# Kernel optimization log

Hardware: AMD Instinct MI355X
Metric: run time of the kernel (lower is better)

Reference implementation:

```python
import jax, jax.numpy as jnp
import numpy as np

B, T, D = 4, 4096, 1024


def setup_inputs() -> dict:
    key = jax.random.key(0)
    ks = jax.random.split(key, 10)
    scale = 1.0 / np.sqrt(D)
    x = jax.random.normal(ks[0], (B, T, D), jnp.float32)
    last_x = jnp.zeros((D,), jnp.float32)
    last_num = jnp.zeros((D,), jnp.float32)
    last_den = jnp.zeros((D,), jnp.float32)
    time_decay = jax.random.normal(ks[1], (D,), jnp.float32) * 0.1
    time_first = jax.random.normal(ks[2], (D,), jnp.float32) * 0.1
    time_mix_k = jax.random.uniform(ks[3], (1, 1, D), jnp.float32)
    time_mix_v = jax.random.uniform(ks[4], (1, 1, D), jnp.float32)
    time_mix_r = jax.random.uniform(ks[5], (1, 1, D), jnp.float32)
    Wk = jax.random.normal(ks[6], (D, D), jnp.float32) * scale
    Wv = jax.random.normal(ks[7], (D, D), jnp.float32) * scale
    Wr = jax.random.normal(ks[8], (D, D), jnp.float32) * scale
    Wo = jax.random.normal(ks[9], (D, D), jnp.float32) * scale
    return {"x": x, "last_x": last_x, "last_num": last_num, "last_den": last_den,
            "time_decay": time_decay, "time_first": time_first,
            "time_mix_k": time_mix_k, "time_mix_v": time_mix_v, "time_mix_r": time_mix_r,
            "Wk": Wk, "Wv": Wv, "Wr": Wr, "Wo": Wo}


def reference(x, last_x, last_num, last_den, time_decay, time_first,
              time_mix_k, time_mix_v, time_mix_r, Wk, Wv, Wr, Wo):
    # token-shift lerps against the incoming state (broadcast over B, T)
    k = jnp.einsum('btd,ed->bte', x * time_mix_k + last_x * (1.0 - time_mix_k), Wk)
    v = jnp.einsum('btd,ed->bte', x * time_mix_v + last_x * (1.0 - time_mix_v), Wv)
    r = jnp.einsum('btd,ed->bte', x * time_mix_r + last_x * (1.0 - time_mix_r), Wr)
    # WKV numerics, exactly as the original (no extra stabilization)
    efk = jnp.exp(time_first + k)          # exp(time_first + k), [B,T,D]
    wkv = (last_num + efk * v) / (last_den + efk)
    rwkv = jax.nn.sigmoid(r) * wkv
    decay = jnp.exp(-jnp.exp(time_decay))  # [D]
    ek = jnp.exp(k)
    num = decay * last_num + ek * v
    den = decay * last_den + ek
    out = jnp.einsum('btd,ed->bte', rwkv, Wo)
    return out, x[..., -1, :], num[..., -1, :], den[..., -1, :]
```

## Files before the change

### kernel.cpp

```cpp
#include <hip/hip_runtime.h>
#include <cstdint>
#include <cstddef>

constexpr int DD = 1024;
constexpr int TT = 4096;
constexpr int BB = 4;
constexpr int MM = BB * TT;

typedef __bf16 bf16x8 __attribute__((ext_vector_type(8)));
typedef float  f32x4  __attribute__((ext_vector_type(4)));

__device__ __forceinline__ unsigned short f2bf(float f) {
  union { float f; uint32_t u; } c; c.f = f;
  uint32_t r = (c.u + 0x7FFFu + ((c.u >> 16) & 1u)) >> 16;
  return (unsigned short)r;
}

__device__ __forceinline__ float fast_rcp(float x) {
  return __builtin_amdgcn_rcpf(x);
}

__device__ __forceinline__ void async_ld16(const unsigned short* g, unsigned short* lds_dst) {
  __builtin_amdgcn_global_load_lds(
      (const __attribute__((address_space(1))) void*)g,
      (__attribute__((address_space(3))) void*)lds_dst,
      16, 0, 0);
}

__global__ void prep_all(const float* __restrict__ Wk, const float* __restrict__ Wv,
                         const float* __restrict__ Wr, const float* __restrict__ Wo,
                         const float* __restrict__ tmk, const float* __restrict__ tmv,
                         const float* __restrict__ tmr,
                         const float* __restrict__ last_x,
                         const float4* __restrict__ x,
                         unsigned short* __restrict__ wz,
                         unsigned short* __restrict__ wo,
                         float* __restrict__ bias,
                         ushort4* __restrict__ xb,
                         float4* __restrict__ out_xlast) {
  if (blockIdx.x < 1024) {
    int w = (blockIdx.x * 256 + threadIdx.x) >> 6;
    int lane = threadIdx.x & 63;
    int z = w >> 10;
    int e = w & (DD - 1);
    const float* W  = (z == 0) ? Wk  : (z == 1) ? Wv  : (z == 2) ? Wr : Wo;
    const float* tm = (z == 0) ? tmk : (z == 1) ? tmv : tmr;
    unsigned short* dst = (z < 3) ? (wz + (size_t)z * DD * DD + (size_t)e * DD)
                                  : (wo + (size_t)e * DD);
    float s = 0.f;
#pragma unroll
    for (int j = 0; j < 4; ++j) {
      int d = j * 256 + lane * 4;
      float4 wv4 = *(const float4*)(W + (size_t)e * DD + d);
      if (z < 3) {
        float4 t4 = *(const float4*)(tm + d);
        float4 l4 = *(const float4*)(last_x + d);
        s += l4.x * (1.f - t4.x) * wv4.x + l4.y * (1.f - t4.y) * wv4.y +
             l4.z * (1.f - t4.z) * wv4.z + l4.w * (1.f - t4.w) * wv4.w;
        wv4.x *= t4.x; wv4.y *= t4.y; wv4.z *= t4.z; wv4.w *= t4.w;
      }
      ushort4 o;
      o.x = f2bf(wv4.x); o.y = f2bf(wv4.y); o.z = f2bf(wv4.z); o.w = f2bf(wv4.w);
      *(ushort4*)(dst + d) = o;
    }
    if (z < 3) {
      for (int off = 32; off; off >>= 1) s += __shfl_down(s, off, 64);
      if (lane == 0) bias[z * DD + e] = s;
    }
  } else {
    int i = (blockIdx.x - 1024) * 256 + threadIdx.x;
    float4 v = x[i];
    ushort4 o;
    o.x = f2bf(v.x); o.y = f2bf(v.y); o.z = f2bf(v.z); o.w = f2bf(v.w);
    xb[i] = o;
    int m = i >> 8;
    if ((m & (TT - 1)) == (TT - 1)) {
      int b = m >> 12;
      out_xlast[b * 256 + (i & 255)] = v;
    }
  }
}

__global__ __launch_bounds__(256, 2) void gemm_kvr(
    const unsigned short* __restrict__ A,
    const unsigned short* __restrict__ Wz,
    const float* __restrict__ bias,
    const float* __restrict__ time_first, const float* __restrict__ time_decay,
    const float* __restrict__ last_num, const float* __restrict__ last_den,
    unsigned short* __restrict__ rwkv,
    float* __restrict__ out_num, float* __restrict__ out_den) {
  __shared__ unsigned short lA[2][128 * 32];
  __shared__ unsigned short lB[2][3][64 * 32];
  const int tid  = threadIdx.x;
  const int lane = tid & 63;
  const int wave = tid >> 6;

  const int id  = blockIdx.y * gridDim.x + blockIdx.x;
  const int xcd = id & 7;
  const int s   = id >> 3;
  const int m0 = (xcd * 16 + (s >> 4)) * 128;
  const int n0 = (s & 15) * 64;

  const int wm = (wave >> 1) * 64;
  const int wn = (wave & 1) * 32;

  f32x4 acc[3][4][2] = {};

  const int fr_row = lane & 15;
  const int fr_kb  = (lane >> 4) * 16;
  const int srow = tid >> 2;
  const int scol = (tid & 3) * 8;

  for (int k0 = 0; k0 < DD; k0 += 64) {
    __syncthreads();
#pragma unroll
    for (int h = 0; h < 2; ++h) {
      int kk = k0 + h * 32;
#pragma unroll
      for (int it = 0; it < 2; ++it) {
        int cc  = it * 256 + tid;
        int row = cc >> 2;
        async_ld16(A + (size_t)(m0 + row) * DD + (kk + scol),
                   lA[h] + (size_t)(it * 256 + wave * 64) * 8);
      }
#pragma unroll
      for (int z = 0; z < 3; ++z) {
        async_ld16(Wz + (size_t)z * DD * DD + (size_t)(n0 + srow) * DD + (kk + scol),
                   lB[h][z] + (size_t)(wave * 64) * 8);
      }
    }
    __syncthreads();

#pragma unroll
    for (int h = 0; h < 2; ++h) {
      bf16x8 af[4], bfr[3][2];
#pragma unroll
      for (int i = 0; i < 4; ++i)
        af[i] = *(const bf16x8*)((const char*)lA[h] + ((wm + i * 16 + fr_row) * 64 + fr_kb));
#pragma unroll
      for (int z = 0; z < 3; ++z)
#pragma unroll
        for (int j = 0; j < 2; ++j)
          bfr[z][j] = *(const bf16x8*)((const char*)lB[h][z] + ((wn + j * 16 + fr_row) * 64 + fr_kb));

#pragma unroll
      for (int mi = 0; mi < 4; ++mi)
#pragma unroll
        for (int z = 0; z < 3; ++z)
#pragma unroll
          for (int ni = 0; ni < 2; ++ni)
            acc[z][mi][ni] = __builtin_amdgcn_mfma_f32_16x16x32_bf16(
                af[mi], bfr[z][ni], acc[z][mi][ni], 0, 0, 0);
    }
  }

  const int crow = (lane >> 4) * 4;
  const int ccol = lane & 15;
#pragma unroll
  for (int ni = 0; ni < 2; ++ni) {
    int gnz = n0 + wn + ni * 16 + ccol;
    float bk = bias[gnz], bv = bias[DD + gnz], br = bias[2 * DD + gnz];
    float tf = time_first[gnz];
    float ln = last_num[gnz], ld = last_den[gnz];
    float dec = __expf(-__expf(time_decay[gnz]));
#pragma unroll
    for (int mi = 0; mi < 4; ++mi) {
#pragma unroll
      for (int r = 0; r < 4; ++r) {
        int gm = m0 + wm + mi * 16 + crow + r;
        float kk = acc[0][mi][ni][r] + bk;
        float vv = acc[1][mi][ni][r] + bv;
        float rr = acc[2][mi][ni][r] + br;
        float efk = __expf(tf + kk);
        float wkv = (ln + efk * vv) * fast_rcp(ld + efk);
        float sr  = fast_rcp(1.0f + __expf(-rr));
        rwkv[(size_t)gm * DD + gnz] = f2bf(sr * wkv);
        if ((gm & (TT - 1)) == (TT - 1)) {
          int b = gm >> 12;
          float ek = __expf(kk);
          out_num[b * DD + gnz] = dec * ln + ek * vv;
          out_den[b * DD + gnz] = dec * ld + ek;
        }
      }
    }
  }
}

__global__ void gemm_bt128(const unsigned short* __restrict__ A,
                           const unsigned short* __restrict__ Bw,
                           float* __restrict__ Cf,
                           int M, int N, int K) {
  __shared__ unsigned short lA[2][128 * 32];
  __shared__ unsigned short lB[2][128 * 32];
  const int tid  = threadIdx.x;
  const int lane = tid & 63;
  const int wave = tid >> 6;

  const int nBlocks = N >> 7;
  const int mBlocks = M >> 7;
  const int id  = blockIdx.y * gridDim.x + blockIdx.x;
  const int xcd = id & 7;
  const int s   = id >> 3;
  const int mPer = mBlocks >> 3;
  const int m0 = (xcd * mPer + s / nBlocks) * 128;
  const int n0 = (s % nBlocks) * 128;

  const int wm = (wave >> 1) * 64;
  const int wn = (wave & 1) * 64;

  f32x4 acc[4][4] = {};
  const int fr_row = lane & 15;
  const int fr_kb  = (lane >> 4) * 16;
  const int scol = (tid & 3) * 8;

  for (int k0 = 0; k0 < K; k0 += 64) {
    __syncthreads();
#pragma unroll
    for (int h = 0; h < 2; ++h) {
      int kk = k0 + h * 32;
#pragma unroll
      for (int it = 0; it < 2; ++it) {
        int cc  = it * 256 + tid;
        int row = cc >> 2;
        async_ld16(A + (size_t)(m0 + row) * K + (kk + scol),
                   lA[h] + (size_t)(it * 256 + wave * 64) * 8);
      }
#pragma unroll
      for (int it = 0; it < 2; ++it) {
        int cc  = it * 256 + tid;
        int row = cc >> 2;
        async_ld16(Bw + (size_t)(n0 + row) * K + (kk + scol),
                   lB[h] + (size_t)(it * 256 + wave * 64) * 8);
      }
    }
    __syncthreads();

#pragma unroll
    for (int h = 0; h < 2; ++h) {
      bf16x8 af[4], bfr[4];
#pragma unroll
      for (int i = 0; i < 4; ++i) {
        af[i]  = *(const bf16x8*)((const char*)lA[h] + ((wm + i * 16 + fr_row) * 64 + fr_kb));
        bfr[i] = *(const bf16x8*)((const char*)lB[h] + ((wn + i * 16 + fr_row) * 64 + fr_kb));
      }
#pragma unroll
      for (int mi = 0; mi < 4; ++mi)
#pragma unroll
        for (int ni = 0; ni < 4; ++ni)
          acc[mi][ni] = __builtin_amdgcn_mfma_f32_16x16x32_bf16(af[mi], bfr[ni], acc[mi][ni], 0, 0, 0);
    }
  }

  const int crow = (lane >> 4) * 4;
  const int ccol = lane & 15;
#pragma unroll
  for (int mi = 0; mi < 4; ++mi) {
#pragma unroll
    for (int ni = 0; ni < 4; ++ni) {
      int gn = n0 + wn + ni * 16 + ccol;
#pragma unroll
      for (int r = 0; r < 4; ++r) {
        int gm = m0 + wm + mi * 16 + crow + r;
        Cf[(size_t)gm * N + gn] = acc[mi][ni][r];
      }
    }
  }
}

extern "C" void kernel_launch(void* const* d_in, const int* in_sizes, int n_in,
                              void* d_out, int out_size, void* d_ws, size_t ws_size,
                              hipStream_t stream) {
  const float* x          = (const float*)d_in[0];
  const float* last_x     = (const float*)d_in[1];
  const float* last_num   = (const float*)d_in[2];
  const float* last_den   = (const float*)d_in[3];
  const float* time_decay = (const float*)d_in[4];
  const float* time_first = (const float*)d_in[5];
  const float* tmk        = (const float*)d_in[6];
  const float* tmv        = (const float*)d_in[7];
  const float* tmr        = (const float*)d_in[8];
  const float* Wk         = (const float*)d_in[9];
  const float* Wv         = (const float*)d_in[10];
  const float* Wr         = (const float*)d_in[11];
  const float* Wo         = (const float*)d_in[12];

  float* out       = (float*)d_out;
  float* out_xlast = out + (size_t)MM * DD;
  float* out_num   = out_xlast + BB * DD;
  float* out_den   = out_num + BB * DD;

  char* ws = (char*)d_ws;
  unsigned short* xb   = (unsigned short*)ws;
  unsigned short* wz   = (unsigned short*)(ws + 33554432);
  unsigned short* wo   = (unsigned short*)(ws + 39845888);
  float*          bias = (float*)(ws + 41943040);
  unsigned short* rwkv = (unsigned short*)(ws + 41955328);

  prep_all<<<1024 + MM * DD / 4 / 256, 256, 0, stream>>>(
      Wk, Wv, Wr, Wo, tmk, tmv, tmr, last_x, (const float4*)x,
      wz, wo, bias, (ushort4*)xb, (float4*)out_xlast);

  gemm_kvr<<<dim3(DD / 64, MM / 128), 256, 0, stream>>>(
      xb, wz, bias, time_first, time_decay, last_num, last_den,
      rwkv, out_num, out_den);

  gemm_bt128<<<dim3(DD / 128, MM / 128), 256, 0, stream>>>(
      rwkv, wo, out, MM, DD, DD);
}
```

Before: 291.5 us.

## Restructure fused KVR GEMM with 512-thread 256-row tiles, swizzled LDS, double-buffered pipeline

The fused k/v/r GEMM moves from 256-thread blocks with 128-row tiles to 512-thread blocks with 256-row tiles. It uses XOR-swizzled LDS layouts to avoid bank conflicts and double-buffers the global-to-LDS async loads so the next k-slice is prefetched while the MFMAs run. The MFMA phases are split per projection, with s_setprio and explicit barriers and waitcnts. The aim is to hide memory latency and reduce LDS conflicts. In exchange, LDS use is larger, register pressure is higher, and the hand-placed synchronisation is fragile.

```diff
diff --git a/kernel.cpp b/kernel.cpp
--- a/kernel.cpp
+++ b/kernel.cpp
@@ -26,6 +26,8 @@
       (__attribute__((address_space(3))) void*)lds_dst,
       16, 0, 0);
 }
+
+__device__ __forceinline__ int swz(int b) { return b ^ (((b >> 9) & 1) << 5); }
 
 __global__ void prep_all(const float* __restrict__ Wk, const float* __restrict__ Wv,
                          const float* __restrict__ Wr, const float* __restrict__ Wo,
@@ -81,7 +83,7 @@
   }
 }
 
-__global__ __launch_bounds__(256, 2) void gemm_kvr(
+__global__ __launch_bounds__(512, 2) void gemm_kvr(
     const unsigned short* __restrict__ A,
     const unsigned short* __restrict__ Wz,
     const float* __restrict__ bias,
@@ -89,8 +91,8 @@
     const float* __restrict__ last_num, const float* __restrict__ last_den,
     unsigned short* __restrict__ rwkv,
     float* __restrict__ out_num, float* __restrict__ out_den) {
-  __shared__ unsigned short lA[2][128 * 32];
-  __shared__ unsigned short lB[2][3][64 * 32];
+  __shared__ __align__(1024) unsigned short lA[2][2][256 * 32];
+  __shared__ __align__(1024) unsigned short lB[2][2][192 * 32];
   const int tid  = threadIdx.x;
   const int lane = tid & 63;
   const int wave = tid >> 6;
@@ -98,64 +100,154 @@
   const int id  = blockIdx.y * gridDim.x + blockIdx.x;
   const int xcd = id & 7;
   const int s   = id >> 3;
-  const int m0 = (xcd * 16 + (s >> 4)) * 128;
+  const int m0 = (xcd * 8 + (s >> 4)) * 256;
   const int n0 = (s & 15) * 64;
 
   const int wm = (wave >> 1) * 64;
   const int wn = (wave & 1) * 32;
+  const int fr = lane & 15;
+  const int fq = lane >> 4;
+
+  int phA[4], phB[3][2];
+#pragma unroll
+  for (int m = 0; m < 4; ++m) phA[m] = swz((wm + m * 16 + fr) * 64 + fq * 16);
+#pragma unroll
+  for (int z = 0; z < 3; ++z)
+#pragma unroll
+    for (int n = 0; n < 2; ++n)
+      phB[z][n] = swz((z * 64 + wn + n * 16 + fr) * 64 + fq * 16);
+
+  size_t offA[2][2];
+  int dstA[2];
+#pragma unroll
+  for (int j = 0; j < 2; ++j) {
+    int i = wave + j * 8;
+    dstA[j] = i * 1024;
+    int pb = i * 1024 + lane * 16;
+    int lq = swz(pb);
+    int r = lq >> 6, cb = lq & 63;
+#pragma unroll
+    for (int kh = 0; kh < 2; ++kh)
+      offA[kh][j] = (size_t)(m0 + r) * DD + kh * 32 + cb / 2;
+  }
+  size_t offB[3];
+  int dstBpl[3], dstBoff[3];
+#pragma unroll
+  for (int t = 0; t < 3; ++t) {
+    int e = wave + t * 8;
+    int kh = (e >= 12) ? 1 : 0;
+    int i = e - 12 * kh;
+    dstBpl[t]  = kh;
+    dstBoff[t] = i * 1024;
+    int pb = i * 1024 + lane * 16;
+    int lq = swz(pb);
+    int r = lq >> 6, cb = lq & 63;
+    int z = r >> 6, zr = r & 63;
+    offB[t] = (size_t)z * DD * DD + (size_t)(n0 + zr) * DD + kh * 32 + cb / 2;
+  }
 
   f32x4 acc[3][4][2] = {};
 
-  const int fr_row = lane & 15;
-  const int fr_kb  = (lane >> 4) * 16;
-  const int srow = tid >> 2;
-  const int scol = (tid & 3) * 8;
-
-  for (int k0 = 0; k0 < DD; k0 += 64) {
-    __syncthreads();
-#pragma unroll
-    for (int h = 0; h < 2; ++h) {
-      int kk = k0 + h * 32;
-#pragma unroll
-      for (int it = 0; it < 2; ++it) {
-        int cc  = it * 256 + tid;
-        int row = cc >> 2;
-        async_ld16(A + (size_t)(m0 + row) * DD + (kk + scol),
-                   lA[h] + (size_t)(it * 256 + wave * 64) * 8);
-      }
-#pragma unroll
-      for (int z = 0; z < 3; ++z) {
-        async_ld16(Wz + (size_t)z * DD * DD + (size_t)(n0 + srow) * DD + (kk + scol),
-                   lB[h][z] + (size_t)(wave * 64) * 8);
-      }
-    }
-    __syncthreads();
-
-#pragma unroll
-    for (int h = 0; h < 2; ++h) {
-      bf16x8 af[4], bfr[3][2];
-#pragma unroll
-      for (int i = 0; i < 4; ++i)
-        af[i] = *(const bf16x8*)((const char*)lA[h] + ((wm + i * 16 + fr_row) * 64 + fr_kb));
-#pragma unroll
-      for (int z = 0; z < 3; ++z)
-#pragma unroll
-        for (int j = 0; j < 2; ++j)
-          bfr[z][j] = *(const bf16x8*)((const char*)lB[h][z] + ((wn + j * 16 + fr_row) * 64 + fr_kb));
-
-#pragma unroll
-      for (int mi = 0; mi < 4; ++mi)
-#pragma unroll
-        for (int z = 0; z < 3; ++z)
-#pragma unroll
-          for (int ni = 0; ni < 2; ++ni)
-            acc[z][mi][ni] = __builtin_amdgcn_mfma_f32_16x16x32_bf16(
-                af[mi], bfr[z][ni], acc[z][mi][ni], 0, 0, 0);
-    }
-  }
-
-  const int crow = (lane >> 4) * 4;
-  const int ccol = lane & 15;
+  auto stage = [&](int pp, int k0e) {
+#pragma unroll
+    for (int kh = 0; kh < 2; ++kh)
+#pragma unroll
+      for (int j = 0; j < 2; ++j)
+        async_ld16(A + offA[kh][j] + k0e,
+                   (unsigned short*)((char*)lA[pp][kh] + dstA[j]));
+#pragma unroll
+    for (int t = 0; t < 3; ++t)
+      async_ld16(Wz + offB[t] + k0e,
+                 (unsigned short*)((char*)lB[pp][dstBpl[t]] + dstBoff[t]));
+  };
+
+  stage(0, 0);
+  asm volatile("s_waitcnt vmcnt(0)" ::: "memory");
+  __builtin_amdgcn_sched_barrier(0);
+  __builtin_amdgcn_s_barrier();
+
+  auto quad = [&](int pp, int k0e, bool do_stage) {
+    bf16x8 af[4][2];
+#pragma unroll
+    for (int ks = 0; ks < 2; ++ks)
+#pragma unroll
+      for (int m = 0; m < 4; ++m)
+        af[m][ks] = *(const bf16x8*)((const char*)lA[pp][ks] + phA[m]);
+    bf16x8 b0[2][2];
+#pragma unroll
+    for (int ks = 0; ks < 2; ++ks)
+#pragma unroll
+      for (int n = 0; n < 2; ++n)
+        b0[n][ks] = *(const bf16x8*)((const char*)lB[pp][ks] + phB[0][n]);
+    if (do_stage) stage(pp ^ 1, k0e + 64);
+    __builtin_amdgcn_s_barrier();
+    asm volatile("s_waitcnt lgkmcnt(0)" ::: "memory");
+    __builtin_amdgcn_sched_barrier(0);
+    __builtin_amdgcn_s_setprio(1);
+#pragma unroll
+    for (int m = 0; m < 4; ++m)
+#pragma unroll
+      for (int n = 0; n < 2; ++n)
+#pragma unroll
+        for (int ks = 0; ks < 2; ++ks)
+          acc[0][m][n] = __builtin_amdgcn_mfma_f32_16x16x32_bf16(
+              af[m][ks], b0[n][ks], acc[0][m][n], 0, 0, 0);
+    __builtin_amdgcn_s_setprio(0);
+    __builtin_amdgcn_s_barrier();
+
+    bf16x8 b1[2][2];
+#pragma unroll
+    for (int ks = 0; ks < 2; ++ks)
+#pragma unroll
+      for (int n = 0; n < 2; ++n)
+        b1[n][ks] = *(const bf16x8*)((const char*)lB[pp][ks] + phB[1][n]);
+    __builtin_amdgcn_s_barrier();
+    asm volatile("s_waitcnt lgkmcnt(0)" ::: "memory");
+    __builtin_amdgcn_sched_barrier(0);
+    __builtin_amdgcn_s_setprio(1);
+#pragma unroll
+    for (int m = 0; m < 4; ++m)
+#pragma unroll
+      for (int n = 0; n < 2; ++n)
+#pragma unroll
+        for (int ks = 0; ks < 2; ++ks)
+          acc[1][m][n] = __builtin_amdgcn_mfma_f32_16x16x32_bf16(
+              af[m][ks], b1[n][ks], acc[1][m][n], 0, 0, 0);
+    __builtin_amdgcn_s_setprio(0);
+    __builtin_amdgcn_s_barrier();
+
+    bf16x8 b2[2][2];
+#pragma unroll
+    for (int ks = 0; ks < 2; ++ks)
+#pragma unroll
+      for (int n = 0; n < 2; ++n)
+        b2[n][ks] = *(const bf16x8*)((const char*)lB[pp][ks] + phB[2][n]);
+    __builtin_amdgcn_s_barrier();
+    asm volatile("s_waitcnt lgkmcnt(0)" ::: "memory");
+    __builtin_amdgcn_sched_barrier(0);
+    __builtin_amdgcn_s_setprio(1);
+#pragma unroll
+    for (int m = 0; m < 4; ++m)
+#pragma unroll
+      for (int n = 0; n < 2; ++n)
+#pragma unroll
+        for (int ks = 0; ks < 2; ++ks)
+          acc[2][m][n] = __builtin_amdgcn_mfma_f32_16x16x32_bf16(
+              af[m][ks], b2[n][ks], acc[2][m][n], 0, 0, 0);
+    __builtin_amdgcn_s_setprio(0);
+    asm volatile("s_waitcnt vmcnt(0)" ::: "memory");
+    __builtin_amdgcn_sched_barrier(0);
+    __builtin_amdgcn_s_barrier();
+  };
+
+#pragma unroll 1
+  for (int kt2 = 0; kt2 < 8; ++kt2) {
+    quad(0, kt2 * 128, true);
+    quad(1, kt2 * 128 + 64, kt2 < 7);
+  }
+
+  const int crow = fq * 4;
+  const int ccol = fr;
 #pragma unroll
   for (int ni = 0; ni < 2; ++ni) {
     int gnz = n0 + wn + ni * 16 + ccol;
@@ -300,7 +392,7 @@
       Wk, Wv, Wr, Wo, tmk, tmv, tmr, last_x, (const float4*)x,
       wz, wo, bias, (ushort4*)xb, (float4*)out_xlast);
 
-  gemm_kvr<<<dim3(DD / 64, MM / 128), 256, 0, stream>>>(
+  gemm_kvr<<<dim3(16, 64), 512, 0, stream>>>(
       xb, wz, bias, time_first, time_decay, last_num, last_den,
       rwkv, out_num, out_den);
 
```

New measurement: 314.3 us. 7.8% more time.

## Pipeline fused KVR GEMM with 4-slot LDS ring, swizzle, and larger tiles

Applied to the files above, without the earlier changes.

The fused K/V/R projection GEMM moves to 512 threads and 256-row M tiles. Its loads now go through a 4-deep LDS ring buffer, issued three stages ahead with explicit vmcnt waits and a single barrier per step, in place of a load-then-compute double sync. LDS addresses are XOR-swizzled to avoid bank conflicts, waves 0-3 load A while waves 4-7 load B, and MFMA runs at raised priority. This is meant to overlap global loads with MFMA and cut sync stalls, at the cost of more LDS per block (about 112 KB) and likely lower occupancy.

```diff
diff --git a/kernel.cpp b/kernel.cpp
--- a/kernel.cpp
+++ b/kernel.cpp
@@ -26,6 +26,8 @@
       (__attribute__((address_space(3))) void*)lds_dst,
       16, 0, 0);
 }
+
+#define VWAIT(n) asm volatile("s_waitcnt vmcnt(" #n ")" ::: "memory")
 
 __global__ void prep_all(const float* __restrict__ Wk, const float* __restrict__ Wv,
                          const float* __restrict__ Wr, const float* __restrict__ Wo,
@@ -81,7 +83,7 @@
   }
 }
 
-__global__ __launch_bounds__(256, 2) void gemm_kvr(
+__global__ __launch_bounds__(512, 2) void gemm_kvr(
     const unsigned short* __restrict__ A,
     const unsigned short* __restrict__ Wz,
     const float* __restrict__ bias,
@@ -89,73 +91,124 @@
     const float* __restrict__ last_num, const float* __restrict__ last_den,
     unsigned short* __restrict__ rwkv,
     float* __restrict__ out_num, float* __restrict__ out_den) {
-  __shared__ unsigned short lA[2][128 * 32];
-  __shared__ unsigned short lB[2][3][64 * 32];
+  __shared__ __align__(1024) unsigned short rA[4][256 * 32];
+  __shared__ __align__(1024) unsigned short rB[4][192 * 32];
   const int tid  = threadIdx.x;
   const int lane = tid & 63;
   const int wave = tid >> 6;
 
   const int id  = blockIdx.y * gridDim.x + blockIdx.x;
   const int xcd = id & 7;
-  const int s   = id >> 3;
-  const int m0 = (xcd * 16 + (s >> 4)) * 128;
-  const int n0 = (s & 15) * 64;
+  const int s_  = id >> 3;
+  const int m0 = (xcd * 8 + (s_ >> 4)) * 256;
+  const int n0 = (s_ & 15) * 64;
 
   const int wm = (wave >> 1) * 64;
   const int wn = (wave & 1) * 32;
+  const int fr = lane & 15;
+  const int fq = lane >> 4;
+
+  int phA[4], phB[3][2];
+#pragma unroll
+  for (int m = 0; m < 4; ++m) {
+    int row = wm + m * 16 + fr;
+    phA[m] = row * 64 + ((fq ^ (row & 3) ^ ((row >> 2) & 3)) << 4);
+  }
+#pragma unroll
+  for (int z = 0; z < 3; ++z)
+#pragma unroll
+    for (int n = 0; n < 2; ++n) {
+      int row = z * 64 + wn + n * 16 + fr;
+      phB[z][n] = row * 64 + ((fq ^ (row & 3) ^ ((row >> 2) & 3)) << 4);
+    }
+
+  const int g_log = (lane & 3) ^ ((lane >> 2) & 3) ^ ((lane >> 4) & 3);
+  size_t srcOff[4];
+  int dstOff[4];
+  if (wave < 4) {
+#pragma unroll
+    for (int j = 0; j < 4; ++j) {
+      int idx = wave * 4 + j;
+      int r = idx * 16 + (lane >> 2);
+      srcOff[j] = (size_t)(m0 + r) * DD + g_log * 8;
+      dstOff[j] = idx * 1024;
+    }
+  } else {
+#pragma unroll
+    for (int j = 0; j < 3; ++j) {
+      int idx = (wave - 4) * 3 + j;
+      int r = idx * 16 + (lane >> 2);
+      int z = r >> 6, zr = r & 63;
+      srcOff[j] = (size_t)z * DD * DD + (size_t)(n0 + zr) * DD + g_log * 8;
+      dstOff[j] = idx * 1024;
+    }
+  }
+
+  auto stage = [&](int slot, int stp) {
+    const int ke = stp * 32;
+    if (wave < 4) {
+#pragma unroll
+      for (int j = 0; j < 4; ++j)
+        async_ld16(A + srcOff[j] + ke, (unsigned short*)((char*)rA[slot] + dstOff[j]));
+    } else {
+#pragma unroll
+      for (int j = 0; j < 3; ++j)
+        async_ld16(Wz + srcOff[j] + ke, (unsigned short*)((char*)rB[slot] + dstOff[j]));
+    }
+  };
 
   f32x4 acc[3][4][2] = {};
 
-  const int fr_row = lane & 15;
-  const int fr_kb  = (lane >> 4) * 16;
-  const int srow = tid >> 2;
-  const int scol = (tid & 3) * 8;
-
-  for (int k0 = 0; k0 < DD; k0 += 64) {
-    __syncthreads();
-#pragma unroll
-    for (int h = 0; h < 2; ++h) {
-      int kk = k0 + h * 32;
-#pragma unroll
-      for (int it = 0; it < 2; ++it) {
-        int cc  = it * 256 + tid;
-        int row = cc >> 2;
-        async_ld16(A + (size_t)(m0 + row) * DD + (kk + scol),
-                   lA[h] + (size_t)(it * 256 + wave * 64) * 8);
-      }
-#pragma unroll
-      for (int z = 0; z < 3; ++z) {
-        async_ld16(Wz + (size_t)z * DD * DD + (size_t)(n0 + srow) * DD + (kk + scol),
-                   lB[h][z] + (size_t)(wave * 64) * 8);
-      }
-    }
-    __syncthreads();
-
-#pragma unroll
-    for (int h = 0; h < 2; ++h) {
-      bf16x8 af[4], bfr[3][2];
-#pragma unroll
-      for (int i = 0; i < 4; ++i)
-        af[i] = *(const bf16x8*)((const char*)lA[h] + ((wm + i * 16 + fr_row) * 64 + fr_kb));
-#pragma unroll
-      for (int z = 0; z < 3; ++z)
-#pragma unroll
-        for (int j = 0; j < 2; ++j)
-          bfr[z][j] = *(const bf16x8*)((const char*)lB[h][z] + ((wn + j * 16 + fr_row) * 64 + fr_kb));
-
-#pragma unroll
-      for (int mi = 0; mi < 4; ++mi)
-#pragma unroll
-        for (int z = 0; z < 3; ++z)
-#pragma unroll
-          for (int ni = 0; ni < 2; ++ni)
-            acc[z][mi][ni] = __builtin_amdgcn_mfma_f32_16x16x32_bf16(
-                af[mi], bfr[z][ni], acc[z][mi][ni], 0, 0, 0);
-    }
-  }
-
-  const int crow = (lane >> 4) * 4;
-  const int ccol = lane & 15;
+  stage(0, 0);
+  stage(1, 1);
+  stage(2, 2);
+  if (wave < 4) VWAIT(8); else VWAIT(6);
+  __builtin_amdgcn_sched_barrier(0);
+  __builtin_amdgcn_s_barrier();
+  __builtin_amdgcn_sched_barrier(0);
+
+#pragma unroll 1
+  for (int s = 0; s < 32; ++s) {
+    const int slot = s & 3;
+    bf16x8 af[4];
+#pragma unroll
+    for (int m = 0; m < 4; ++m)
+      af[m] = *(const bf16x8*)((const char*)rA[slot] + phA[m]);
+    bf16x8 bfr[3][2];
+#pragma unroll
+    for (int z = 0; z < 3; ++z)
+#pragma unroll
+      for (int n = 0; n < 2; ++n)
+        bfr[z][n] = *(const bf16x8*)((const char*)rB[slot] + phB[z][n]);
+
+    if (s < 29) stage((s + 3) & 3, s + 3);
+
+    __builtin_amdgcn_s_barrier();
+    asm volatile("s_waitcnt lgkmcnt(0)" ::: "memory");
+    __builtin_amdgcn_sched_barrier(0);
+    __builtin_amdgcn_s_setprio(1);
+#pragma unroll
+    for (int z = 0; z < 3; ++z)
+#pragma unroll
+      for (int m = 0; m < 4; ++m)
+#pragma unroll
+        for (int n = 0; n < 2; ++n)
+          acc[z][m][n] = __builtin_amdgcn_mfma_f32_16x16x32_bf16(
+              af[m], bfr[z][n], acc[z][m][n], 0, 0, 0);
+    __builtin_amdgcn_s_setprio(0);
+
+    if (s < 31) {
+      if (s < 29)       { if (wave < 4) VWAIT(8); else VWAIT(6); }
+      else if (s == 29) { if (wave < 4) VWAIT(4); else VWAIT(3); }
+      else              { VWAIT(0); }
+      __builtin_amdgcn_sched_barrier(0);
+      __builtin_amdgcn_s_barrier();
+      __builtin_amdgcn_sched_barrier(0);
+    }
+  }
+
+  const int crow = fq * 4;
+  const int ccol = fr;
 #pragma unroll
   for (int ni = 0; ni < 2; ++ni) {
     int gnz = n0 + wn + ni * 16 + ccol;
@@ -300,7 +353,7 @@
       Wk, Wv, Wr, Wo, tmk, tmv, tmr, last_x, (const float4*)x,
       wz, wo, bias, (ushort4*)xb, (float4*)out_xlast);
 
-  gemm_kvr<<<dim3(DD / 64, MM / 128), 256, 0, stream>>>(
+  gemm_kvr<<<dim3(16, 64), 512, 0, stream>>>(
       xb, wz, bias, time_first, time_decay, last_num, last_den,
       rwkv, out_num, out_den);
 
```

Result: slower. 335.3 us (+15.0%).

## Add 4-stage async LDS pipeline with XOR swizzle to both GEMMs

Applied to the files above, without the earlier changes.

Both GEMM kernels drop the load-all-then-compute loop with two __syncthreads per 64-wide K step. They now use a 4-slot ring of 32-wide K tiles, issuing async global-to-LDS loads three tiles ahead and waiting on vmcnt counters before a single barrier per iteration. An XOR swizzle on the LDS byte offsets, applied at load and fragment read, aims to cut bank conflicts on the bf16x8 reads. This costs twice the LDS per block, which may reduce occupancy, and relies on hand-written waitcnt values matching the number of loads in flight.

```diff
diff --git a/kernel.cpp b/kernel.cpp
--- a/kernel.cpp
+++ b/kernel.cpp
@@ -26,6 +26,12 @@
       (__attribute__((address_space(3))) void*)lds_dst,
       16, 0, 0);
 }
+
+#define VWAIT(n) asm volatile("s_waitcnt vmcnt(" #n ")" ::: "memory")
+#define LWAIT0() asm volatile("s_waitcnt lgkmcnt(0)" ::: "memory")
+#define SB()     __builtin_amdgcn_sched_barrier(0)
+
+__device__ __forceinline__ int swzb(int b) { return b ^ (((b >> 9) & 1) << 5); }
 
 __global__ void prep_all(const float* __restrict__ Wk, const float* __restrict__ Wv,
                          const float* __restrict__ Wr, const float* __restrict__ Wo,
@@ -89,8 +95,8 @@
     const float* __restrict__ last_num, const float* __restrict__ last_den,
     unsigned short* __restrict__ rwkv,
     float* __restrict__ out_num, float* __restrict__ out_den) {
-  __shared__ unsigned short lA[2][128 * 32];
-  __shared__ unsigned short lB[2][3][64 * 32];
+  __shared__ __align__(1024) unsigned short sA[4][128 * 32];
+  __shared__ __align__(1024) unsigned short sB[4][3 * 64 * 32];
   const int tid  = threadIdx.x;
   const int lane = tid & 63;
   const int wave = tid >> 6;
@@ -103,59 +109,98 @@
 
   const int wm = (wave >> 1) * 64;
   const int wn = (wave & 1) * 32;
+  const int fr = lane & 15;
+  const int fq = lane >> 4;
+
+  int phA[4], phB[3][2];
+#pragma unroll
+  for (int m = 0; m < 4; ++m)
+    phA[m] = swzb((wm + m * 16 + fr) * 64 + fq * 16);
+#pragma unroll
+  for (int z = 0; z < 3; ++z)
+#pragma unroll
+    for (int n = 0; n < 2; ++n)
+      phB[z][n] = swzb(z * 4096 + (wn + n * 16 + fr) * 64 + fq * 16);
+
+  size_t aSrc[2]; int aDst[2];
+#pragma unroll
+  for (int it = 0; it < 2; ++it) {
+    int plane = it * 4 + wave;
+    aDst[it] = plane * 1024;
+    int pb = plane * 1024 + lane * 16;
+    int lq = swzb(pb);
+    int r = lq >> 6, cb = lq & 63;
+    aSrc[it] = (size_t)(m0 + r) * DD + (cb >> 1);
+  }
+  size_t bSrc[3]; int bDst[3];
+#pragma unroll
+  for (int j = 0; j < 3; ++j) {
+    int base = j * 4096 + wave * 1024;
+    bDst[j] = base;
+    int pb = base + lane * 16;
+    int lq = swzb(pb);
+    int r = lq >> 6, cb = lq & 63;
+    int z = r >> 6, zr = r & 63;
+    bSrc[j] = (size_t)z * DD * DD + (size_t)(n0 + zr) * DD + (cb >> 1);
+  }
+
+  auto stage = [&](int slot, int tile) {
+    const int kk = tile * 32;
+#pragma unroll
+    for (int it = 0; it < 2; ++it)
+      async_ld16(A + aSrc[it] + kk, (unsigned short*)((char*)sA[slot] + aDst[it]));
+#pragma unroll
+    for (int j = 0; j < 3; ++j)
+      async_ld16(Wz + bSrc[j] + kk, (unsigned short*)((char*)sB[slot] + bDst[j]));
+  };
 
   f32x4 acc[3][4][2] = {};
 
-  const int fr_row = lane & 15;
-  const int fr_kb  = (lane >> 4) * 16;
-  const int srow = tid >> 2;
-  const int scol = (tid & 3) * 8;
-
-  for (int k0 = 0; k0 < DD; k0 += 64) {
-    __syncthreads();
-#pragma unroll
-    for (int h = 0; h < 2; ++h) {
-      int kk = k0 + h * 32;
-#pragma unroll
-      for (int it = 0; it < 2; ++it) {
-        int cc  = it * 256 + tid;
-        int row = cc >> 2;
-        async_ld16(A + (size_t)(m0 + row) * DD + (kk + scol),
-                   lA[h] + (size_t)(it * 256 + wave * 64) * 8);
-      }
-#pragma unroll
-      for (int z = 0; z < 3; ++z) {
-        async_ld16(Wz + (size_t)z * DD * DD + (size_t)(n0 + srow) * DD + (kk + scol),
-                   lB[h][z] + (size_t)(wave * 64) * 8);
-      }
-    }
-    __syncthreads();
-
-#pragma unroll
-    for (int h = 0; h < 2; ++h) {
-      bf16x8 af[4], bfr[3][2];
-#pragma unroll
-      for (int i = 0; i < 4; ++i)
-        af[i] = *(const bf16x8*)((const char*)lA[h] + ((wm + i * 16 + fr_row) * 64 + fr_kb));
+  stage(0, 0);
+  stage(1, 1);
+  stage(2, 2);
+  VWAIT(10); SB();
+  __builtin_amdgcn_s_barrier();
+  SB();
+
+#pragma unroll 1
+  for (int t = 0; t < 32; ++t) {
+    const int slot = t & 3;
+    if (t < 29) stage((t + 3) & 3, t + 3);
+    SB();
+
+    bf16x8 af[4], bfr[3][2];
+#pragma unroll
+    for (int m = 0; m < 4; ++m)
+      af[m] = *(const bf16x8*)((const char*)sA[slot] + phA[m]);
+#pragma unroll
+    for (int z = 0; z < 3; ++z)
+#pragma unroll
+      for (int n = 0; n < 2; ++n)
+        bfr[z][n] = *(const bf16x8*)((const char*)sB[slot] + phB[z][n]);
+
+#pragma unroll
+    for (int mi = 0; mi < 4; ++mi)
 #pragma unroll
       for (int z = 0; z < 3; ++z)
 #pragma unroll
-        for (int j = 0; j < 2; ++j)
-          bfr[z][j] = *(const bf16x8*)((const char*)lB[h][z] + ((wn + j * 16 + fr_row) * 64 + fr_kb));
-
-#pragma unroll
-      for (int mi = 0; mi < 4; ++mi)
-#pragma unroll
-        for (int z = 0; z < 3; ++z)
-#pragma unroll
-          for (int ni = 0; ni < 2; ++ni)
-            acc[z][mi][ni] = __builtin_amdgcn_mfma_f32_16x16x32_bf16(
-                af[mi], bfr[z][ni], acc[z][mi][ni], 0, 0, 0);
-    }
-  }
-
-  const int crow = (lane >> 4) * 4;
-  const int ccol = lane & 15;
+        for (int ni = 0; ni < 2; ++ni)
+          acc[z][mi][ni] = __builtin_amdgcn_mfma_f32_16x16x32_bf16(
+              af[mi], bfr[z][ni], acc[z][mi][ni], 0, 0, 0);
+
+    if (t < 31) {
+      LWAIT0();
+      if (t < 29)       VWAIT(10);
+      else if (t == 29) VWAIT(5);
+      else              VWAIT(0);
+      SB();
+      __builtin_amdgcn_s_barrier();
+      SB();
+    }
+  }
+
+  const int crow = fq * 4;
+  const int ccol = fr;
 #pragma unroll
   for (int ni = 0; ni < 2; ++ni) {
     int gnz = n0 + wn + ni * 16 + ccol;
@@ -190,8 +235,8 @@
                            const unsigned short* __restrict__ Bw,
                            float* __restrict__ Cf,
                            int M, int N, int K) {
-  __shared__ unsigned short lA[2][128 * 32];
-  __shared__ unsigned short lB[2][128 * 32];
+  __shared__ __align__(1024) unsigned short sA[4][128 * 32];
+  __shared__ __align__(1024) unsigned short sB[4][128 * 32];
   const int tid  = threadIdx.x;
   const int lane = tid & 63;
   const int wave = tid >> 6;
@@ -207,52 +252,79 @@
 
   const int wm = (wave >> 1) * 64;
   const int wn = (wave & 1) * 64;
+  const int fr = lane & 15;
+  const int fq = lane >> 4;
+
+  int phA[4], phB[4];
+#pragma unroll
+  for (int i = 0; i < 4; ++i) {
+    phA[i] = swzb((wm + i * 16 + fr) * 64 + fq * 16);
+    phB[i] = swzb((wn + i * 16 + fr) * 64 + fq * 16);
+  }
+
+  size_t aSrc[2], bSrc[2]; int dstO[2];
+#pragma unroll
+  for (int it = 0; it < 2; ++it) {
+    int plane = it * 4 + wave;
+    dstO[it] = plane * 1024;
+    int pb = plane * 1024 + lane * 16;
+    int lq = swzb(pb);
+    int r = lq >> 6, cb = lq & 63;
+    aSrc[it] = (size_t)(m0 + r) * K + (cb >> 1);
+    bSrc[it] = (size_t)(n0 + r) * K + (cb >> 1);
+  }
+
+  auto stage = [&](int slot, int tile) {
+    const int kk = tile * 32;
+#pragma unroll
+    for (int it = 0; it < 2; ++it)
+      async_ld16(A + aSrc[it] + kk, (unsigned short*)((char*)sA[slot] + dstO[it]));
+#pragma unroll
+    for (int it = 0; it < 2; ++it)
+      async_ld16(Bw + bSrc[it] + kk, (unsigned short*)((char*)sB[slot] + dstO[it]));
+  };
 
   f32x4 acc[4][4] = {};
-  const int fr_row = lane & 15;
-  const int fr_kb  = (lane >> 4) * 16;
-  const int scol = (tid & 3) * 8;
-
-  for (int k0 = 0; k0 < K; k0 += 64) {
-    __syncthreads();
-#pragma unroll
-    for (int h = 0; h < 2; ++h) {
-      int kk = k0 + h * 32;
-#pragma unroll
-      for (int it = 0; it < 2; ++it) {
-        int cc  = it * 256 + tid;
-        int row = cc >> 2;
-        async_ld16(A + (size_t)(m0 + row) * K + (kk + scol),
-                   lA[h] + (size_t)(it * 256 + wave * 64) * 8);
-      }
-#pragma unroll
-      for (int it = 0; it < 2; ++it) {
-        int cc  = it * 256 + tid;
-        int row = cc >> 2;
-        async_ld16(Bw + (size_t)(n0 + row) * K + (kk + scol),
-                   lB[h] + (size_t)(it * 256 + wave * 64) * 8);
-      }
-    }
-    __syncthreads();
-
-#pragma unroll
-    for (int h = 0; h < 2; ++h) {
-      bf16x8 af[4], bfr[4];
-#pragma unroll
-      for (int i = 0; i < 4; ++i) {
-        af[i]  = *(const bf16x8*)((const char*)lA[h] + ((wm + i * 16 + fr_row) * 64 + fr_kb));
-        bfr[i] = *(const bf16x8*)((const char*)lB[h] + ((wn + i * 16 + fr_row) * 64 + fr_kb));
-      }
-#pragma unroll
-      for (int mi = 0; mi < 4; ++mi)
-#pragma unroll
-        for (int ni = 0; ni < 4; ++ni)
-          acc[mi][ni] = __builtin_amdgcn_mfma_f32_16x16x32_bf16(af[mi], bfr[ni], acc[mi][ni], 0, 0, 0);
-    }
-  }
-
-  const int crow = (lane >> 4) * 4;
-  const int ccol = lane & 15;
+  const int nt = K >> 5;
+
+  stage(0, 0);
+  stage(1, 1);
+  stage(2, 2);
+  VWAIT(8); SB();
+  __builtin_amdgcn_s_barrier();
+  SB();
+
+#pragma unroll 1
+  for (int t = 0; t < nt; ++t) {
+    const int slot = t & 3;
+    if (t + 3 < nt) stage((t + 3) & 3, t + 3);
+    SB();
+
+    bf16x8 af[4], bfr[4];
+#pragma unroll
+    for (int i = 0; i < 4; ++i) {
+      af[i]  = *(const bf16x8*)((const char*)sA[slot] + phA[i]);
+      bfr[i] = *(const bf16x8*)((const char*)sB[slot] + phB[i]);
+    }
+#pragma unroll
+    for (int mi = 0; mi < 4; ++mi)
+#pragma unroll
+      for (int ni = 0; ni < 4; ++ni)
+        acc[mi][ni] = __builtin_amdgcn_mfma_f32_16x16x32_bf16(af[mi], bfr[ni], acc[mi][ni], 0, 0, 0);
+
+    if (t < nt - 1) {
+      LWAIT0();
+      if (t < nt - 3)       VWAIT(8);
+      else if (t == nt - 3) VWAIT(4);
+      else                  VWAIT(0);
+      SB();
+      __builtin_amdgcn_s_barrier();
+      SB();
+    }
+  }
+
+  const int crow = fq * 4;
+  const int ccol = fr;
 #pragma unroll
   for (int mi = 0; mi < 4; ++mi) {
 #pragma unroll
```

After: 313.9 us. +7.7%, slower.
